# Kernel tuning notes

Hardware: AMD Instinct MI355X
Metric: run time of the kernel (lower is better)

## Reference

```python
import jax, jax.numpy as jnp
import numpy as np

DIM = 384
NUM_HEADS = 12
WS = 8            # window_size
SS = 4            # shift_size
HEAD_DIM = DIM // NUM_HEADS
SCALE = HEAD_DIM ** -0.5
N = WS * WS       # tokens per window
EPS = 1e-5
MLP_HIDDEN = 4 * DIM

# relative position index (static, matches torch buffer construction)
_coords = np.stack(np.meshgrid(np.arange(WS), np.arange(WS), indexing='ij')).reshape(2, -1)
_rel = (_coords[:, :, None] - _coords[:, None, :]).transpose(1, 2, 0)  # [N,N,2]
_rel[..., 0] += WS - 1
_rel[..., 1] += WS - 1
_rel[..., 0] *= 2 * WS - 1
RPI = jnp.asarray(_rel.sum(-1))  # [N,N] int


def layer_norm(x, g, b):
    m = x.mean(-1, keepdims=True)
    v = ((x - m) ** 2).mean(-1, keepdims=True)
    return (x - m) / jnp.sqrt(v + EPS) * g + b


def window_partition(x):
    B, Hh, Ww, C = x.shape
    x = x.reshape(B, Hh // WS, WS, Ww // WS, WS, C).transpose(0, 1, 3, 2, 4, 5)
    return x.reshape(-1, WS, WS, C)


def window_reverse(w, Hh, Ww):
    B = w.shape[0] // ((Hh // WS) * (Ww // WS))
    x = w.reshape(B, Hh // WS, Ww // WS, WS, WS, -1).transpose(0, 1, 3, 2, 4, 5)
    return x.reshape(B, Hh, Ww, -1)


def attention_mask(Hp, Wp):
    # region id along each axis: 0 = [0, Hp-WS), 1 = [Hp-WS, Hp-SS), 2 = [Hp-SS, Hp)
    h_id = np.zeros(Hp, np.int32); h_id[Hp - WS:Hp - SS] = 1; h_id[Hp - SS:] = 2
    w_id = np.zeros(Wp, np.int32); w_id[Wp - WS:Wp - SS] = 1; w_id[Wp - SS:] = 2
    cnt = h_id[:, None] * 3 + w_id[None, :]                      # [Hp, Wp]
    img = jnp.asarray(cnt, jnp.float32).reshape(1, Hp, Wp, 1)
    mw = window_partition(img).reshape(-1, N)                    # [nW, N]
    am = mw[:, None, :] - mw[:, :, None]                         # [nW, N, N]
    return jnp.where(am != 0, jnp.float32(-100.0), jnp.float32(0.0))


def setup_inputs() -> dict:
    key = jax.random.key(0)
    ks = jax.random.split(key, 8)
    B, H, W = 32, 64, 64
    std = 0.02
    return {
        'x': jax.random.normal(ks[0], (B, H * W, DIM), jnp.float32),
        'qkv_w': jax.random.normal(ks[1], (DIM, 3 * DIM), jnp.float32) * std,
        'qkv_b': jnp.zeros((3 * DIM,), jnp.float32),
        'proj_w': jax.random.normal(ks[2], (DIM, DIM), jnp.float32) * std,
        'proj_b': jnp.zeros((DIM,), jnp.float32),
        'rpb_table': jax.random.normal(ks[3], ((2 * WS - 1) * (2 * WS - 1), NUM_HEADS), jnp.float32) * std,
        'n1_g': jnp.ones((DIM,), jnp.float32), 'n1_b': jnp.zeros((DIM,), jnp.float32),
        'n2_g': jnp.ones((DIM,), jnp.float32), 'n2_b': jnp.zeros((DIM,), jnp.float32),
        'fc1_w': jax.random.normal(ks[4], (DIM, MLP_HIDDEN), jnp.float32) * std,
        'fc1_b': jnp.zeros((MLP_HIDDEN,), jnp.float32),
        'fc2_w': jax.random.normal(ks[5], (MLP_HIDDEN, DIM), jnp.float32) * std,
        'fc2_b': jnp.zeros((DIM,), jnp.float32),
        'H': 64, 'W': 64,
    }


def reference(x, qkv_w, qkv_b, proj_w, proj_b, rpb_table, n1_g, n1_b, n2_g, n2_b,
              fc1_w, fc1_b, fc2_w, fc2_b, H, W):
    B, L, C = x.shape
    shortcut = x
    h = layer_norm(x, n1_g, n1_b).reshape(B, H, W, C)
    pad_r = (WS - W % WS) % WS
    pad_b = (WS - H % WS) % WS
    if pad_r or pad_b:
        h = jnp.pad(h, ((0, 0), (0, pad_b), (0, pad_r), (0, 0)))
    Hp, Wp = H + pad_b, W + pad_r
    shifted = jnp.roll(h, shift=(-SS, -SS), axis=(1, 2))
    xw = window_partition(shifted).reshape(-1, N, C)             # [B_, N, C]
    B_ = xw.shape[0]

    qkv = (xw @ qkv_w + qkv_b).reshape(B_, N, 3, NUM_HEADS, HEAD_DIM)
    q = qkv[:, :, 0].transpose(0, 2, 1, 3) * SCALE               # [B_, h, N, d]
    k = qkv[:, :, 1].transpose(0, 2, 1, 3)
    v = qkv[:, :, 2].transpose(0, 2, 1, 3)

    attn = jnp.einsum('bhnd,bhmd->bhnm', q, k)                   # [B_, h, N, N]
    bias = rpb_table[RPI].transpose(2, 0, 1)                     # [h, N, N]
    attn = attn + bias[None]

    mask = attention_mask(Hp, Wp)                                # [nW, N, N]
    nW = mask.shape[0]
    attn = attn.reshape(B_ // nW, nW, NUM_HEADS, N, N) + mask[None, :, None]
    attn = jax.nn.softmax(attn.reshape(B_, NUM_HEADS, N, N), axis=-1)

    out = jnp.einsum('bhnm,bhmd->bhnd', attn, v)
    out = out.transpose(0, 2, 1, 3).reshape(B_, N, C)
    out = out @ proj_w + proj_b

    out = window_reverse(out.reshape(-1, WS, WS, C), Hp, Wp)
    out = jnp.roll(out, shift=(SS, SS), axis=(1, 2))
    out = out[:, :H, :W, :].reshape(B, H * W, C)

    x = shortcut + out
    h2 = layer_norm(x, n2_g, n2_b)
    mlp = jax.nn.gelu(h2 @ fc1_w + fc1_b, approximate=False) @ fc2_w + fc2_b
    return x + mlp
```

## Files before the change

### kernel.cpp

```cpp
#include <hip/hip_runtime.h>
#include <math.h>


#define ROWS_TOTAL 131072
#define NWIN_TOTAL 2048

typedef __attribute__((ext_vector_type(8))) __bf16 bf16x8;
typedef __attribute__((ext_vector_type(4))) float f32x4;
typedef __attribute__((ext_vector_type(8))) unsigned short ushort8;

__device__ __forceinline__ unsigned short f2bf(float f) {
  unsigned u = __builtin_bit_cast(unsigned, f);
  u = (u + 0x7fffu + ((u >> 16) & 1u)) >> 16;
  return (unsigned short)u;
}

__device__ __forceinline__ void gload16(const void* g, void* l) {
  __builtin_amdgcn_global_load_lds(
      (const __attribute__((address_space(1))) unsigned int*)g,
      (__attribute__((address_space(3))) unsigned int*)l, 16, 0, 0);
}

__device__ __forceinline__ int gather_row(int win, int t) {
  int b = win >> 6, wi = (win >> 3) & 7, wj = win & 7;
  int gi = (wi * 8 + (t >> 3) + 4) & 63;
  int gj = (wj * 8 + (t & 7) + 4) & 63;
  return (b << 12) + (gi << 6) + gj;
}

__device__ __forceinline__ void frag_mma(const ushort* As_, const ushort* Bs_,
                                         int wr, int wc, int lane,
                                         f32x4 acc[8][4]) {
  const int go = (((lane >> 4) ^ ((lane >> 1) & 3)) << 3);
  const int lr = lane & 15;
  bf16x8 bfr[4];
#pragma unroll
  for (int nj = 0; nj < 4; ++nj)
    bfr[nj] = *(const bf16x8*)(Bs_ + (wc * 64 + nj * 16 + lr) * 32 + go);
#pragma unroll
  for (int mi = 0; mi < 8; ++mi) {
    bf16x8 af = *(const bf16x8*)(As_ + (wr * 128 + mi * 16 + lr) * 32 + go);
#pragma unroll
    for (int nj = 0; nj < 4; ++nj)
      acc[mi][nj] = __builtin_amdgcn_mfma_f32_16x16x32_bf16(
          af, bfr[nj], acc[mi][nj], 0, 0, 0);
  }
}

#define VM6() asm volatile("s_waitcnt vmcnt(6)" ::: "memory")
#define VM0() asm volatile("s_waitcnt vmcnt(0)" ::: "memory")
#define SCB() __builtin_amdgcn_sched_barrier(0)
#define BARR() __builtin_amdgcn_s_barrier()

#define STG(B_, T_)                                    \
  { size_t ko = (size_t)(T_) * 64;                     \
    gload16(aS0 + ko, &As[B_][aD]);                    \
    gload16(aS1 + ko, &As[B_][aD + 512]);              \
    gload16(aS2 + ko, &As[B_][aD + 1024]);             \
    gload16(aS3 + ko, &As[B_][aD + 1536]);             \
    gload16(bS0 + ko, &Bs[B_][bD]);                    \
    gload16(bS1 + ko, &Bs[B_][bD + 512]); }

#define GEMM_PIPE(NK)                                               \
  {                                                                 \
    STG(0, 0);                                                      \
    STG(1, 1);                                                      \
    VM6(); SCB(); BARR(); SCB();                                    \
    int cur = 0;                                                    \
    for (int t = 0; t < (NK); ++t) {                                \
      if (t + 2 < (NK)) {                                           \
        int nb = cur + 2; if (nb >= 3) nb -= 3;                     \
        STG(nb, t + 2);                                             \
      }                                                             \
      __builtin_amdgcn_s_setprio(1);                                \
      frag_mma(&As[cur][0], &Bs[cur][0], wr, wc, lane, acc);        \
      __builtin_amdgcn_s_setprio(0);                                \
      if (t + 2 < (NK)) { VM6(); } else { VM0(); }                  \
      SCB(); BARR(); SCB();                                         \
      ++cur; if (cur == 3) cur = 0;                                 \
    }                                                               \
  }

__global__ __launch_bounds__(256) void wprep_k(
    const float* __restrict__ qkvw, const float* __restrict__ projw,
    const float* __restrict__ fc1w, const float* __restrict__ fc2w,
    ushort* __restrict__ wq, ushort* __restrict__ wp,
    ushort* __restrict__ w1, ushort* __restrict__ w2) {
  int gid = blockIdx.x * 256 + threadIdx.x;
  const int S1 = 1152 * 384;
  const int S2 = S1 + 384 * 384;
  const int S3 = S2 + 1536 * 384;
  const int S4 = S3 + 384 * 1536;
  if (gid < S1) {
    int n = gid / 384, k = gid - n * 384;
    wq[gid] = f2bf(qkvw[(size_t)k * 1152 + n]);
  } else if (gid < S2) {
    int i = gid - S1, n = i / 384, k = i - n * 384;
    wp[i] = f2bf(projw[(size_t)k * 384 + n]);
  } else if (gid < S3) {
    int i = gid - S2, n = i / 384, k = i - n * 384;
    w1[i] = f2bf(fc1w[(size_t)k * 1536 + n]);
  } else if (gid < S4) {
    int i = gid - S3, n = i / 1536, k = i - n * 1536;
    w2[i] = f2bf(fc2w[(size_t)k * 384 + n]);
  }
}

__global__ __launch_bounds__(256) void ln_fused_k(
    const float* __restrict__ x, const float* __restrict__ g,
    const float* __restrict__ b, ushort* __restrict__ o) {
  int wid = threadIdx.x >> 6, lane = threadIdx.x & 63;
  int row = (blockIdx.x << 2) + wid;
  const float* p = x + (size_t)row * 384;
  float2 v[3];
  float s = 0.f, ss = 0.f;
#pragma unroll
  for (int c = 0; c < 3; ++c) {
    v[c] = *(const float2*)(p + lane * 2 + c * 128);
    s += v[c].x + v[c].y;
    ss += v[c].x * v[c].x + v[c].y * v[c].y;
  }
#pragma unroll
  for (int off = 1; off < 64; off <<= 1) {
    s += __shfl_xor(s, off);
    ss += __shfl_xor(ss, off);
  }
  float m = s * (1.f / 384.f);
  float r = rsqrtf(ss * (1.f / 384.f) - m * m + 1e-5f);
  ushort* op = o + (size_t)row * 384;
#pragma unroll
  for (int c = 0; c < 3; ++c) {
    float2 gg = *(const float2*)(g + lane * 2 + c * 128);
    float2 bb = *(const float2*)(b + lane * 2 + c * 128);
    union { ushort u[2]; unsigned w; } pk;
    pk.u[0] = f2bf((v[c].x - m) * r * gg.x + bb.x);
    pk.u[1] = f2bf((v[c].y - m) * r * gg.y + bb.y);
    *(unsigned*)(op + lane * 2 + c * 128) = pk.w;
  }
}

__global__ __launch_bounds__(256, 2) void qkv_mfma_k(
    const ushort* __restrict__ xln, const ushort* __restrict__ wq,
    const float* __restrict__ qkvb, float* __restrict__ qd,
    float* __restrict__ kd, float* __restrict__ vd, int wc0) {
  __shared__ __align__(16) ushort As[3][8192];
  __shared__ __align__(16) ushort Bs[3][4096];
  __shared__ int rowS[256];
  const int tid = threadIdx.x;
  const int w = tid >> 6, lane = tid & 63;
  const int wr = w >> 1, wc = w & 1;
  const int bm = blockIdx.x, n0 = blockIdx.y * 128;
  {
    int win = wc0 + bm * 4 + (tid >> 6);
    rowS[tid] = gather_row(win, tid & 63);
  }
  __syncthreads();
  const int sle = (((lane & 3) ^ ((lane >> 3) & 3)) << 4);
  const int rb = w * 64 + (lane >> 2);
  const char* aS0 = (const char*)xln + (size_t)rowS[rb] * 768 + sle;
  const char* aS1 = (const char*)xln + (size_t)rowS[rb + 16] * 768 + sle;
  const char* aS2 = (const char*)xln + (size_t)rowS[rb + 32] * 768 + sle;
  const char* aS3 = (const char*)xln + (size_t)rowS[rb + 48] * 768 + sle;
  const int nb = n0 + w * 32 + (lane >> 2);
  const char* bS0 = (const char*)wq + (size_t)nb * 768 + sle;
  const char* bS1 = (const char*)wq + (size_t)(nb + 16) * 768 + sle;
  const int aD = w * 2048 + lane * 8;
  const int bD = w * 1024 + lane * 8;
  f32x4 acc[8][4];
#pragma unroll
  for (int i = 0; i < 8; ++i)
#pragma unroll
    for (int j = 0; j < 4; ++j) acc[i][j] = (f32x4)(0.f);
  GEMM_PIPE(12);
  const float scale = 0.17677669529663687f;
#pragma unroll
  for (int mi = 0; mi < 8; ++mi) {
#pragma unroll
    for (int r = 0; r < 4; ++r) {
      int rr = wr * 128 + mi * 16 + ((lane >> 4) << 2) + r;
      int w_rel = bm * 4 + (rr >> 6), t = rr & 63;
#pragma unroll
      for (int nj = 0; nj < 4; ++nj) {
        int nc = n0 + wc * 64 + nj * 16 + (lane & 15);
        float v = acc[mi][nj][r] + qkvb[nc];
        int qi = nc / 384, rem = nc - qi * 384;
        int hh = rem >> 5, d = rem & 31;
        float* base = (qi == 0) ? qd : (qi == 1 ? kd : vd);
        if (qi == 0) v *= scale;
        base[(((size_t)w_rel * 12 + hh) << 11) + (t << 5) + d] = v;
      }
    }
  }
}

__global__ __launch_bounds__(128) void attn_k(
    const float* __restrict__ q, const float* __restrict__ k,
    const float* __restrict__ v, const float* __restrict__ rpb,
    ushort* __restrict__ ao, int wc0) {
  __shared__ __align__(16) float kbuf[2][64][32];
  __shared__ __align__(16) float vbuf[2][64][32];
  __shared__ float bias[2][232];
  __shared__ int region[64];
  const int tid = threadIdx.x;
  const int wid = tid >> 6, lane = tid & 63;
  const int w = blockIdx.x, win = wc0 + w;
  const int head = blockIdx.y * 2 + wid;
  if (tid < 64) {
    int wi = (win >> 3) & 7, wj = win & 7;
    int pi = wi * 8 + (tid >> 3), pj = wj * 8 + (tid & 7);
    int ri = pi < 56 ? 0 : (pi < 60 ? 1 : 2);
    int rj = pj < 56 ? 0 : (pj < 60 ? 1 : 2);
    region[tid] = ri * 3 + rj;
  }
  const size_t hb = ((size_t)w * 12 + head) * 2048;
  const float* kp = k + hb;
  const float* vp = v + hb;
#pragma unroll
  for (int s = 0; s < 8; ++s) {
    int f = s * 64 + lane;
    int r = f >> 3, c = (f & 7) << 2;
    *(float4*)&kbuf[wid][r][c] = *(const float4*)(kp + r * 32 + c);
    *(float4*)&vbuf[wid][r][c] = *(const float4*)(vp + r * 32 + c);
  }
  for (int s = lane; s < 225; s += 64) bias[wid][s] = rpb[s * 12 + head];
  __syncthreads();
  const int i = lane;
  float qr[32];
  const float* qp = q + hb + (i << 5);
#pragma unroll
  for (int c = 0; c < 32; c += 4) {
    float4 t4 = *(const float4*)(qp + c);
    qr[c] = t4.x; qr[c + 1] = t4.y; qr[c + 2] = t4.z; qr[c + 3] = t4.w;
  }
  const int yi = i >> 3, xi = i & 7, regi = region[i];
  float sc[64];
  float mx = -3.0e38f;
#pragma unroll
  for (int j = 0; j < 64; ++j) {
    float a = 0.f;
#pragma unroll
    for (int c = 0; c < 32; c += 4) {
      float4 kv = *(float4*)&kbuf[wid][j][c];
      a = fmaf(qr[c], kv.x, a);
      a = fmaf(qr[c + 1], kv.y, a);
      a = fmaf(qr[c + 2], kv.z, a);
      a = fmaf(qr[c + 3], kv.w, a);
    }
    int dy = yi - (j >> 3) + 7, dx = xi - (j & 7) + 7;
    a += bias[wid][dy * 15 + dx];
    if (region[j] != regi) a -= 100.f;
    sc[j] = a;
    mx = fmaxf(mx, a);
  }
  float sum = 0.f;
#pragma unroll
  for (int j = 0; j < 64; ++j) {
    float e = __expf(sc[j] - mx);
    sc[j] = e;
    sum += e;
  }
  const float inv = 1.f / sum;
  float o[32];
#pragma unroll
  for (int c = 0; c < 32; ++c) o[c] = 0.f;
#pragma unroll
  for (int j = 0; j < 64; ++j) {
    float p = sc[j];
#pragma unroll
    for (int c = 0; c < 32; c += 4) {
      float4 vv = *(float4*)&vbuf[wid][j][c];
      o[c] = fmaf(p, vv.x, o[c]);
      o[c + 1] = fmaf(p, vv.y, o[c + 1]);
      o[c + 2] = fmaf(p, vv.z, o[c + 2]);
      o[c + 3] = fmaf(p, vv.w, o[c + 3]);
    }
  }
  ushort* op = ao + ((size_t)(w * 64 + i)) * 384 + (head << 5);
#pragma unroll
  for (int c = 0; c < 32; c += 8) {
    ushort8 pk;
#pragma unroll
    for (int j2 = 0; j2 < 8; ++j2) pk[j2] = f2bf(o[c + j2] * inv);
    *(ushort8*)(op + c) = pk;
  }
}

__global__ __launch_bounds__(256, 2) void proj_mfma_k(
    const ushort* __restrict__ ao, const ushort* __restrict__ wp,
    const float* __restrict__ pb, const float* __restrict__ x,
    float* __restrict__ x2, int wc0) {
  __shared__ __align__(16) ushort As[3][8192];
  __shared__ __align__(16) ushort Bs[3][4096];
  const int tid = threadIdx.x;
  const int w = tid >> 6, lane = tid & 63;
  const int wr = w >> 1, wc = w & 1;
  const int bm = blockIdx.x, n0 = blockIdx.y * 128;
  const int sle = (((lane & 3) ^ ((lane >> 3) & 3)) << 4);
  const int rb = bm * 256 + w * 64 + (lane >> 2);
  const char* aS0 = (const char*)ao + (size_t)rb * 768 + sle;
  const char* aS1 = aS0 + (size_t)16 * 768;
  const char* aS2 = aS0 + (size_t)32 * 768;
  const char* aS3 = aS0 + (size_t)48 * 768;
  const int nb = n0 + w * 32 + (lane >> 2);
  const char* bS0 = (const char*)wp + (size_t)nb * 768 + sle;
  const char* bS1 = (const char*)wp + (size_t)(nb + 16) * 768 + sle;
  const int aD = w * 2048 + lane * 8;
  const int bD = w * 1024 + lane * 8;
  f32x4 acc[8][4];
#pragma unroll
  for (int i = 0; i < 8; ++i)
#pragma unroll
    for (int j = 0; j < 4; ++j) acc[i][j] = (f32x4)(0.f);
  GEMM_PIPE(12);
#pragma unroll
  for (int mi = 0; mi < 8; ++mi) {
#pragma unroll
    for (int r = 0; r < 4; ++r) {
      int rr = wr * 128 + mi * 16 + ((lane >> 4) << 2) + r;
      int gl = bm * 256 + rr;
      int gr = gather_row(wc0 + (gl >> 6), gl & 63);
#pragma unroll
      for (int nj = 0; nj < 4; ++nj) {
        int nc = n0 + wc * 64 + nj * 16 + (lane & 15);
        size_t idx = (size_t)gr * 384 + nc;
        x2[idx] = acc[mi][nj][r] + pb[nc] + x[idx];
      }
    }
  }
}

__global__ __launch_bounds__(256, 2) void fc1_mfma_k(
    const ushort* __restrict__ x2ln, const ushort* __restrict__ w1,
    const float* __restrict__ fb, ushort* __restrict__ hm, int row0) {
  __shared__ __align__(16) ushort As[3][8192];
  __shared__ __align__(16) ushort Bs[3][4096];
  const int tid = threadIdx.x;
  const int w = tid >> 6, lane = tid & 63;
  const int wr = w >> 1, wc = w & 1;
  const int bm = blockIdx.x, n0 = blockIdx.y * 128;
  const int sle = (((lane & 3) ^ ((lane >> 3) & 3)) << 4);
  const int rb = row0 + bm * 256 + w * 64 + (lane >> 2);
  const char* aS0 = (const char*)x2ln + (size_t)rb * 768 + sle;
  const char* aS1 = aS0 + (size_t)16 * 768;
  const char* aS2 = aS0 + (size_t)32 * 768;
  const char* aS3 = aS0 + (size_t)48 * 768;
  const int nb = n0 + w * 32 + (lane >> 2);
  const char* bS0 = (const char*)w1 + (size_t)nb * 768 + sle;
  const char* bS1 = (const char*)w1 + (size_t)(nb + 16) * 768 + sle;
  const int aD = w * 2048 + lane * 8;
  const int bD = w * 1024 + lane * 8;
  f32x4 acc[8][4];
#pragma unroll
  for (int i = 0; i < 8; ++i)
#pragma unroll
    for (int j = 0; j < 4; ++j) acc[i][j] = (f32x4)(0.f);
  GEMM_PIPE(12);
#pragma unroll
  for (int mi = 0; mi < 8; ++mi) {
#pragma unroll
    for (int r = 0; r < 4; ++r) {
      int rr = wr * 128 + mi * 16 + ((lane >> 4) << 2) + r;
      size_t lrow = (size_t)(bm * 256 + rr);
#pragma unroll
      for (int nj = 0; nj < 4; ++nj) {
        int nc = n0 + wc * 64 + nj * 16 + (lane & 15);
        float v = acc[mi][nj][r] + fb[nc];
        v = 0.5f * v * (1.f + erff(v * 0.70710678118654752f));
        hm[lrow * 1536 + nc] = f2bf(v);
      }
    }
  }
}

__global__ __launch_bounds__(256, 2) void fc2_mfma_k(
    const ushort* __restrict__ hm, const ushort* __restrict__ w2,
    const float* __restrict__ fb, float* __restrict__ out, int row0) {
  __shared__ __align__(16) ushort As[3][8192];
  __shared__ __align__(16) ushort Bs[3][4096];
  const int tid = threadIdx.x;
  const int w = tid >> 6, lane = tid & 63;
  const int wr = w >> 1, wc = w & 1;
  const int bm = blockIdx.x, n0 = blockIdx.y * 128;
  const int sle = (((lane & 3) ^ ((lane >> 3) & 3)) << 4);
  const int rb = bm * 256 + w * 64 + (lane >> 2);
  const char* aS0 = (const char*)hm + (size_t)rb * 3072 + sle;
  const char* aS1 = aS0 + (size_t)16 * 3072;
  const char* aS2 = aS0 + (size_t)32 * 3072;
  const char* aS3 = aS0 + (size_t)48 * 3072;
  const int nb = n0 + w * 32 + (lane >> 2);
  const char* bS0 = (const char*)w2 + (size_t)nb * 3072 + sle;
  const char* bS1 = (const char*)w2 + (size_t)(nb + 16) * 3072 + sle;
  const int aD = w * 2048 + lane * 8;
  const int bD = w * 1024 + lane * 8;
  f32x4 acc[8][4];
#pragma unroll
  for (int i = 0; i < 8; ++i)
#pragma unroll
    for (int j = 0; j < 4; ++j) acc[i][j] = (f32x4)(0.f);
  GEMM_PIPE(48);
#pragma unroll
  for (int mi = 0; mi < 8; ++mi) {
#pragma unroll
    for (int r = 0; r < 4; ++r) {
      int rr = wr * 128 + mi * 16 + ((lane >> 4) << 2) + r;
      size_t grow = (size_t)(row0 + bm * 256 + rr);
#pragma unroll
      for (int nj = 0; nj < 4; ++nj) {
        int nc = n0 + wc * 64 + nj * 16 + (lane & 15);
        size_t idx = grow * 384 + nc;
        out[idx] = out[idx] + acc[mi][nj][r] + fb[nc];
      }
    }
  }
}

extern "C" void kernel_launch(void* const* d_in, const int* in_sizes, int n_in,
                              void* d_out, int out_size, void* d_ws, size_t ws_size,
                              hipStream_t stream) {
  const float* x = (const float*)d_in[0];
  const float* qkv_w = (const float*)d_in[1];
  const float* qkv_b = (const float*)d_in[2];
  const float* proj_w = (const float*)d_in[3];
  const float* proj_b = (const float*)d_in[4];
  const float* rpb = (const float*)d_in[5];
  const float* n1g = (const float*)d_in[6];
  const float* n1b = (const float*)d_in[7];
  const float* n2g = (const float*)d_in[8];
  const float* n2b = (const float*)d_in[9];
  const float* fc1w = (const float*)d_in[10];
  const float* fc1b = (const float*)d_in[11];
  const float* fc2w = (const float*)d_in[12];
  const float* fc2b = (const float*)d_in[13];
  float* out = (float*)d_out;
  char* ws = (char*)d_ws;

  ushort* wq = (ushort*)ws;
  ushort* wp = wq + 442368;
  ushort* w1 = wp + 147456;
  ushort* w2 = w1 + 589824;
  ushort* xln = (ushort*)(ws + 3538944);
  char* scratch = ws + 3538944 + 100663296;
  size_t base = 3538944 + 100663296;
  size_t ssz = (ws_size > base) ? ws_size - base : 0;

  wprep_k<<<6912, 256, 0, stream>>>(qkv_w, proj_w, fc1w, fc2w, wq, wp, w1, w2);
  ln_fused_k<<<ROWS_TOTAL / 4, 256, 0, stream>>>(x, n1g, n1b, xln);

  const size_t perwin = 344064;
  int nwc = (int)(ssz / perwin);
  if (nwc > NWIN_TOTAL) nwc = NWIN_TOTAL;
  nwc &= ~3;
  if (nwc < 4) nwc = 4;
  float* qd = (float*)scratch;
  float* kd = qd + (size_t)nwc * 24576;
  float* vd = kd + (size_t)nwc * 24576;
  ushort* ao = (ushort*)(vd + (size_t)nwc * 24576);
  for (int wc0 = 0; wc0 < NWIN_TOTAL; wc0 += nwc) {
    int nw = (NWIN_TOTAL - wc0 < nwc) ? (NWIN_TOTAL - wc0) : nwc;
    qkv_mfma_k<<<dim3(nw / 4, 9), 256, 0, stream>>>(xln, wq, qkv_b, qd, kd, vd, wc0);
    attn_k<<<dim3(nw, 6), 128, 0, stream>>>(qd, kd, vd, rpb, ao, wc0);
    proj_mfma_k<<<dim3(nw / 4, 3), 256, 0, stream>>>(ao, wp, proj_b, x, out, wc0);
  }

  ln_fused_k<<<ROWS_TOTAL / 4, 256, 0, stream>>>(out, n2g, n2b, xln);
  const size_t pergrp = 786432;
  int ngc = (int)(ssz / pergrp);
  if (ngc > 512) ngc = 512;
  if (ngc < 1) ngc = 1;
  ushort* hm = (ushort*)scratch;
  for (int g0 = 0; g0 < 512; g0 += ngc) {
    int ng = (512 - g0 < ngc) ? (512 - g0) : ngc;
    fc1_mfma_k<<<dim3(ng, 12), 256, 0, stream>>>(xln, w1, fc1b, hm, g0 * 256);
    fc2_mfma_k<<<dim3(ng, 3), 256, 0, stream>>>(hm, w2, fc2b, out, g0 * 256);
  }
}
```

Measured before the change: 1.600 ms.

## Load GEMM fragments directly from global into registers; store QKV as bf16

Replaces the LDS triple-buffered global_load_lds pipeline in all four GEMMs with direct per-lane global loads of MFMA fragments into registers, double-buffered over K steps. Stores Q/K/V intermediates as bf16 instead of fp32, halving scratch traffic and letting more windows fit per chunk. Swaps the grid dimensions so N-tiles vary fastest, which should improve reuse of the A operand in L2. The risks are that dropping LDS sharing means each wave fetches its own operands from global/L2 with less coalescing, that register pressure rises, and that bf16 Q/K/V slightly reduces precision.

```diff
diff --git a/kernel.cpp b/kernel.cpp
--- a/kernel.cpp
+++ b/kernel.cpp
@@ -14,11 +14,8 @@
   u = (u + 0x7fffu + ((u >> 16) & 1u)) >> 16;
   return (unsigned short)u;
 }
-
-__device__ __forceinline__ void gload16(const void* g, void* l) {
-  __builtin_amdgcn_global_load_lds(
-      (const __attribute__((address_space(1))) unsigned int*)g,
-      (__attribute__((address_space(3))) unsigned int*)l, 16, 0, 0);
+__device__ __forceinline__ float bf2f(unsigned short u) {
+  return __builtin_bit_cast(float, (unsigned)u << 16);
 }
 
 __device__ __forceinline__ int gather_row(int win, int t) {
@@ -28,57 +25,45 @@
   return (b << 12) + (gi << 6) + gj;
 }
 
-__device__ __forceinline__ void frag_mma(const ushort* As_, const ushort* Bs_,
-                                         int wr, int wc, int lane,
-                                         f32x4 acc[8][4]) {
-  const int go = (((lane >> 4) ^ ((lane >> 1) & 3)) << 3);
-  const int lr = lane & 15;
-  bf16x8 bfr[4];
-#pragma unroll
-  for (int nj = 0; nj < 4; ++nj)
-    bfr[nj] = *(const bf16x8*)(Bs_ + (wc * 64 + nj * 16 + lr) * 32 + go);
-#pragma unroll
-  for (int mi = 0; mi < 8; ++mi) {
-    bf16x8 af = *(const bf16x8*)(As_ + (wr * 128 + mi * 16 + lr) * 32 + go);
-#pragma unroll
-    for (int nj = 0; nj < 4; ++nj)
-      acc[mi][nj] = __builtin_amdgcn_mfma_f32_16x16x32_bf16(
-          af, bfr[nj], acc[mi][nj], 0, 0, 0);
-  }
-}
-
-#define VM6() asm volatile("s_waitcnt vmcnt(6)" ::: "memory")
-#define VM0() asm volatile("s_waitcnt vmcnt(0)" ::: "memory")
-#define SCB() __builtin_amdgcn_sched_barrier(0)
-#define BARR() __builtin_amdgcn_s_barrier()
-
-#define STG(B_, T_)                                    \
-  { size_t ko = (size_t)(T_) * 64;                     \
-    gload16(aS0 + ko, &As[B_][aD]);                    \
-    gload16(aS1 + ko, &As[B_][aD + 512]);              \
-    gload16(aS2 + ko, &As[B_][aD + 1024]);             \
-    gload16(aS3 + ko, &As[B_][aD + 1536]);             \
-    gload16(bS0 + ko, &Bs[B_][bD]);                    \
-    gload16(bS1 + ko, &Bs[B_][bD + 512]); }
-
-#define GEMM_PIPE(NK)                                               \
-  {                                                                 \
-    STG(0, 0);                                                      \
-    STG(1, 1);                                                      \
-    VM6(); SCB(); BARR(); SCB();                                    \
-    int cur = 0;                                                    \
-    for (int t = 0; t < (NK); ++t) {                                \
-      if (t + 2 < (NK)) {                                           \
-        int nb = cur + 2; if (nb >= 3) nb -= 3;                     \
-        STG(nb, t + 2);                                             \
-      }                                                             \
-      __builtin_amdgcn_s_setprio(1);                                \
-      frag_mma(&As[cur][0], &Bs[cur][0], wr, wc, lane, acc);        \
-      __builtin_amdgcn_s_setprio(0);                                \
-      if (t + 2 < (NK)) { VM6(); } else { VM0(); }                  \
-      SCB(); BARR(); SCB();                                         \
-      ++cur; if (cur == 3) cur = 0;                                 \
-    }                                                               \
+#define MFMA_SET(AF, BF)                                                   \
+  _Pragma("unroll") for (int mi = 0; mi < 8; ++mi)                         \
+  _Pragma("unroll") for (int nj = 0; nj < 4; ++nj)                         \
+      acc[mi][nj] = __builtin_amdgcn_mfma_f32_16x16x32_bf16(               \
+          AF[mi], BF[nj], acc[mi][nj], 0, 0, 0);
+
+#define REG_PIPE(NK)                                                       \
+  {                                                                        \
+    bf16x8 a0[8], b0[4], a1[8], b1[4];                                     \
+    _Pragma("unroll") for (int i = 0; i < 8; ++i)                          \
+        a0[i] = *(const bf16x8*)aP[i];                                     \
+    _Pragma("unroll") for (int j = 0; j < 4; ++j)                          \
+        b0[j] = *(const bf16x8*)bP[j];                                     \
+    _Pragma("unroll") for (int i = 0; i < 8; ++i)                          \
+        a1[i] = *(const bf16x8*)(aP[i] + 32);                              \
+    _Pragma("unroll") for (int j = 0; j < 4; ++j)                          \
+        b1[j] = *(const bf16x8*)(bP[j] + 32);                              \
+    for (int t = 0; t < (NK) - 2; t += 2) {                                \
+      _Pragma("unroll") for (int i = 0; i < 8; ++i) aP[i] += 64;           \
+      _Pragma("unroll") for (int j = 0; j < 4; ++j) bP[j] += 64;           \
+      __builtin_amdgcn_s_setprio(1);                                       \
+      MFMA_SET(a0, b0);                                                    \
+      __builtin_amdgcn_s_setprio(0);                                       \
+      _Pragma("unroll") for (int i = 0; i < 8; ++i)                        \
+          a0[i] = *(const bf16x8*)aP[i];                                   \
+      _Pragma("unroll") for (int j = 0; j < 4; ++j)                        \
+          b0[j] = *(const bf16x8*)bP[j];                                   \
+      __builtin_amdgcn_s_setprio(1);                                       \
+      MFMA_SET(a1, b1);                                                    \
+      __builtin_amdgcn_s_setprio(0);                                       \
+      _Pragma("unroll") for (int i = 0; i < 8; ++i)                        \
+          a1[i] = *(const bf16x8*)(aP[i] + 32);                            \
+      _Pragma("unroll") for (int j = 0; j < 4; ++j)                        \
+          b1[j] = *(const bf16x8*)(bP[j] + 32);                            \
+    }                                                                      \
+    __builtin_amdgcn_s_setprio(1);                                         \
+    MFMA_SET(a0, b0);                                                      \
+    MFMA_SET(a1, b1);                                                      \
+    __builtin_amdgcn_s_setprio(0);                                         \
   }
 
 __global__ __launch_bounds__(256) void wprep_k(
@@ -141,37 +126,30 @@
 
 __global__ __launch_bounds__(256, 2) void qkv_mfma_k(
     const ushort* __restrict__ xln, const ushort* __restrict__ wq,
-    const float* __restrict__ qkvb, float* __restrict__ qd,
-    float* __restrict__ kd, float* __restrict__ vd, int wc0) {
-  __shared__ __align__(16) ushort As[3][8192];
-  __shared__ __align__(16) ushort Bs[3][4096];
-  __shared__ int rowS[256];
+    const float* __restrict__ qkvb, ushort* __restrict__ qd,
+    ushort* __restrict__ kd, ushort* __restrict__ vd, int wc0) {
   const int tid = threadIdx.x;
   const int w = tid >> 6, lane = tid & 63;
   const int wr = w >> 1, wc = w & 1;
-  const int bm = blockIdx.x, n0 = blockIdx.y * 128;
-  {
-    int win = wc0 + bm * 4 + (tid >> 6);
-    rowS[tid] = gather_row(win, tid & 63);
-  }
-  __syncthreads();
-  const int sle = (((lane & 3) ^ ((lane >> 3) & 3)) << 4);
-  const int rb = w * 64 + (lane >> 2);
-  const char* aS0 = (const char*)xln + (size_t)rowS[rb] * 768 + sle;
-  const char* aS1 = (const char*)xln + (size_t)rowS[rb + 16] * 768 + sle;
-  const char* aS2 = (const char*)xln + (size_t)rowS[rb + 32] * 768 + sle;
-  const char* aS3 = (const char*)xln + (size_t)rowS[rb + 48] * 768 + sle;
-  const int nb = n0 + w * 32 + (lane >> 2);
-  const char* bS0 = (const char*)wq + (size_t)nb * 768 + sle;
-  const char* bS1 = (const char*)wq + (size_t)(nb + 16) * 768 + sle;
-  const int aD = w * 2048 + lane * 8;
-  const int bD = w * 1024 + lane * 8;
+  const int n0 = blockIdx.x * 128, bm = blockIdx.y;
+  const int lr = lane & 15, kch = (lane >> 4) * 8;
+  const ushort* aP[8];
+#pragma unroll
+  for (int i = 0; i < 8; ++i) {
+    int rr = wr * 128 + i * 16 + lr;
+    int gr = gather_row(wc0 + bm * 4 + (rr >> 6), rr & 63);
+    aP[i] = xln + (size_t)gr * 384 + kch;
+  }
+  const ushort* bP[4];
+#pragma unroll
+  for (int j = 0; j < 4; ++j)
+    bP[j] = wq + (size_t)(n0 + wc * 64 + j * 16 + lr) * 384 + kch;
   f32x4 acc[8][4];
 #pragma unroll
   for (int i = 0; i < 8; ++i)
 #pragma unroll
     for (int j = 0; j < 4; ++j) acc[i][j] = (f32x4)(0.f);
-  GEMM_PIPE(12);
+  REG_PIPE(12);
   const float scale = 0.17677669529663687f;
 #pragma unroll
   for (int mi = 0; mi < 8; ++mi) {
@@ -185,17 +163,17 @@
         float v = acc[mi][nj][r] + qkvb[nc];
         int qi = nc / 384, rem = nc - qi * 384;
         int hh = rem >> 5, d = rem & 31;
-        float* base = (qi == 0) ? qd : (qi == 1 ? kd : vd);
+        ushort* base = (qi == 0) ? qd : (qi == 1 ? kd : vd);
         if (qi == 0) v *= scale;
-        base[(((size_t)w_rel * 12 + hh) << 11) + (t << 5) + d] = v;
+        base[(((size_t)w_rel * 12 + hh) << 11) + (t << 5) + d] = f2bf(v);
       }
     }
   }
 }
 
 __global__ __launch_bounds__(128) void attn_k(
-    const float* __restrict__ q, const float* __restrict__ k,
-    const float* __restrict__ v, const float* __restrict__ rpb,
+    const ushort* __restrict__ q, const ushort* __restrict__ k,
+    const ushort* __restrict__ v, const float* __restrict__ rpb,
     ushort* __restrict__ ao, int wc0) {
   __shared__ __align__(16) float kbuf[2][64][32];
   __shared__ __align__(16) float vbuf[2][64][32];
@@ -213,24 +191,30 @@
     region[tid] = ri * 3 + rj;
   }
   const size_t hb = ((size_t)w * 12 + head) * 2048;
-  const float* kp = k + hb;
-  const float* vp = v + hb;
-#pragma unroll
-  for (int s = 0; s < 8; ++s) {
+  const ushort* kp = k + hb;
+  const ushort* vp = v + hb;
+#pragma unroll
+  for (int s = 0; s < 4; ++s) {
     int f = s * 64 + lane;
-    int r = f >> 3, c = (f & 7) << 2;
-    *(float4*)&kbuf[wid][r][c] = *(const float4*)(kp + r * 32 + c);
-    *(float4*)&vbuf[wid][r][c] = *(const float4*)(vp + r * 32 + c);
+    int r = f >> 2, c = (f & 3) * 8;
+    ushort8 ku = *(const ushort8*)(kp + r * 32 + c);
+    ushort8 vu = *(const ushort8*)(vp + r * 32 + c);
+#pragma unroll
+    for (int j = 0; j < 8; ++j) {
+      kbuf[wid][r][c + j] = bf2f(ku[j]);
+      vbuf[wid][r][c + j] = bf2f(vu[j]);
+    }
   }
   for (int s = lane; s < 225; s += 64) bias[wid][s] = rpb[s * 12 + head];
   __syncthreads();
   const int i = lane;
   float qr[32];
-  const float* qp = q + hb + (i << 5);
-#pragma unroll
-  for (int c = 0; c < 32; c += 4) {
-    float4 t4 = *(const float4*)(qp + c);
-    qr[c] = t4.x; qr[c + 1] = t4.y; qr[c + 2] = t4.z; qr[c + 3] = t4.w;
+  const ushort* qp = q + hb + (i << 5);
+#pragma unroll
+  for (int c = 0; c < 4; ++c) {
+    ushort8 qu = *(const ushort8*)(qp + c * 8);
+#pragma unroll
+    for (int j = 0; j < 8; ++j) qr[c * 8 + j] = bf2f(qu[j]);
   }
   const int yi = i >> 3, xi = i & 7, regi = region[i];
   float sc[64];
@@ -289,29 +273,25 @@
     const ushort* __restrict__ ao, const ushort* __restrict__ wp,
     const float* __restrict__ pb, const float* __restrict__ x,
     float* __restrict__ x2, int wc0) {
-  __shared__ __align__(16) ushort As[3][8192];
-  __shared__ __align__(16) ushort Bs[3][4096];
   const int tid = threadIdx.x;
   const int w = tid >> 6, lane = tid & 63;
   const int wr = w >> 1, wc = w & 1;
-  const int bm = blockIdx.x, n0 = blockIdx.y * 128;
-  const int sle = (((lane & 3) ^ ((lane >> 3) & 3)) << 4);
-  const int rb = bm * 256 + w * 64 + (lane >> 2);
-  const char* aS0 = (const char*)ao + (size_t)rb * 768 + sle;
-  const char* aS1 = aS0 + (size_t)16 * 768;
-  const char* aS2 = aS0 + (size_t)32 * 768;
-  const char* aS3 = aS0 + (size_t)48 * 768;
-  const int nb = n0 + w * 32 + (lane >> 2);
-  const char* bS0 = (const char*)wp + (size_t)nb * 768 + sle;
-  const char* bS1 = (const char*)wp + (size_t)(nb + 16) * 768 + sle;
-  const int aD = w * 2048 + lane * 8;
-  const int bD = w * 1024 + lane * 8;
+  const int n0 = blockIdx.x * 128, bm = blockIdx.y;
+  const int lr = lane & 15, kch = (lane >> 4) * 8;
+  const ushort* aP[8];
+#pragma unroll
+  for (int i = 0; i < 8; ++i)
+    aP[i] = ao + (size_t)(bm * 256 + wr * 128 + i * 16 + lr) * 384 + kch;
+  const ushort* bP[4];
+#pragma unroll
+  for (int j = 0; j < 4; ++j)
+    bP[j] = wp + (size_t)(n0 + wc * 64 + j * 16 + lr) * 384 + kch;
   f32x4 acc[8][4];
 #pragma unroll
   for (int i = 0; i < 8; ++i)
 #pragma unroll
     for (int j = 0; j < 4; ++j) acc[i][j] = (f32x4)(0.f);
-  GEMM_PIPE(12);
+  REG_PIPE(12);
 #pragma unroll
   for (int mi = 0; mi < 8; ++mi) {
 #pragma unroll
@@ -332,29 +312,25 @@
 __global__ __launch_bounds__(256, 2) void fc1_mfma_k(
     const ushort* __restrict__ x2ln, const ushort* __restrict__ w1,
     const float* __restrict__ fb, ushort* __restrict__ hm, int row0) {
-  __shared__ __align__(16) ushort As[3][8192];
-  __shared__ __align__(16) ushort Bs[3][4096];
   const int tid = threadIdx.x;
   const int w = tid >> 6, lane = tid & 63;
   const int wr = w >> 1, wc = w & 1;
-  const int bm = blockIdx.x, n0 = blockIdx.y * 128;
-  const int sle = (((lane & 3) ^ ((lane >> 3) & 3)) << 4);
-  const int rb = row0 + bm * 256 + w * 64 + (lane >> 2);
-  const char* aS0 = (const char*)x2ln + (size_t)rb * 768 + sle;
-  const char* aS1 = aS0 + (size_t)16 * 768;
-  const char* aS2 = aS0 + (size_t)32 * 768;
-  const char* aS3 = aS0 + (size_t)48 * 768;
-  const int nb = n0 + w * 32 + (lane >> 2);
-  const char* bS0 = (const char*)w1 + (size_t)nb * 768 + sle;
-  const char* bS1 = (const char*)w1 + (size_t)(nb + 16) * 768 + sle;
-  const int aD = w * 2048 + lane * 8;
-  const int bD = w * 1024 + lane * 8;
+  const int n0 = blockIdx.x * 128, bm = blockIdx.y;
+  const int lr = lane & 15, kch = (lane >> 4) * 8;
+  const ushort* aP[8];
+#pragma unroll
+  for (int i = 0; i < 8; ++i)
+    aP[i] = x2ln + (size_t)(row0 + bm * 256 + wr * 128 + i * 16 + lr) * 384 + kch;
+  const ushort* bP[4];
+#pragma unroll
+  for (int j = 0; j < 4; ++j)
+    bP[j] = w1 + (size_t)(n0 + wc * 64 + j * 16 + lr) * 384 + kch;
   f32x4 acc[8][4];
 #pragma unroll
   for (int i = 0; i < 8; ++i)
 #pragma unroll
     for (int j = 0; j < 4; ++j) acc[i][j] = (f32x4)(0.f);
-  GEMM_PIPE(12);
+  REG_PIPE(12);
 #pragma unroll
   for (int mi = 0; mi < 8; ++mi) {
 #pragma unroll
@@ -364,9 +340,9 @@
 #pragma unroll
       for (int nj = 0; nj < 4; ++nj) {
         int nc = n0 + wc * 64 + nj * 16 + (lane & 15);
-        float v = acc[mi][nj][r] + fb[nc];
-        v = 0.5f * v * (1.f + erff(v * 0.70710678118654752f));
-        hm[lrow * 1536 + nc] = f2bf(v);
+        float vv = acc[mi][nj][r] + fb[nc];
+        vv = 0.5f * vv * (1.f + erff(vv * 0.70710678118654752f));
+        hm[lrow * 1536 + nc] = f2bf(vv);
       }
     }
   }
@@ -375,29 +351,25 @@
 __global__ __launch_bounds__(256, 2) void fc2_mfma_k(
     const ushort* __restrict__ hm, const ushort* __restrict__ w2,
     const float* __restrict__ fb, float* __restrict__ out, int row0) {
-  __shared__ __align__(16) ushort As[3][8192];
-  __shared__ __align__(16) ushort Bs[3][4096];
   const int tid = threadIdx.x;
   const int w = tid >> 6, lane = tid & 63;
   const int wr = w >> 1, wc = w & 1;
-  const int bm = blockIdx.x, n0 = blockIdx.y * 128;
-  const int sle = (((lane & 3) ^ ((lane >> 3) & 3)) << 4);
-  const int rb = bm * 256 + w * 64 + (lane >> 2);
-  const char* aS0 = (const char*)hm + (size_t)rb * 3072 + sle;
-  const char* aS1 = aS0 + (size_t)16 * 3072;
-  const char* aS2 = aS0 + (size_t)32 * 3072;
-  const char* aS3 = aS0 + (size_t)48 * 3072;
-  const int nb = n0 + w * 32 + (lane >> 2);
-  const char* bS0 = (const char*)w2 + (size_t)nb * 3072 + sle;
-  const char* bS1 = (const char*)w2 + (size_t)(nb + 16) * 3072 + sle;
-  const int aD = w * 2048 + lane * 8;
-  const int bD = w * 1024 + lane * 8;
+  const int n0 = blockIdx.x * 128, bm = blockIdx.y;
+  const int lr = lane & 15, kch = (lane >> 4) * 8;
+  const ushort* aP[8];
+#pragma unroll
+  for (int i = 0; i < 8; ++i)
+    aP[i] = hm + (size_t)(bm * 256 + wr * 128 + i * 16 + lr) * 1536 + kch;
+  const ushort* bP[4];
+#pragma unroll
+  for (int j = 0; j < 4; ++j)
+    bP[j] = w2 + (size_t)(n0 + wc * 64 + j * 16 + lr) * 1536 + kch;
   f32x4 acc[8][4];
 #pragma unroll
   for (int i = 0; i < 8; ++i)
 #pragma unroll
     for (int j = 0; j < 4; ++j) acc[i][j] = (f32x4)(0.f);
-  GEMM_PIPE(48);
+  REG_PIPE(48);
 #pragma unroll
   for (int mi = 0; mi < 8; ++mi) {
 #pragma unroll
@@ -446,20 +418,20 @@
   wprep_k<<<6912, 256, 0, stream>>>(qkv_w, proj_w, fc1w, fc2w, wq, wp, w1, w2);
   ln_fused_k<<<ROWS_TOTAL / 4, 256, 0, stream>>>(x, n1g, n1b, xln);
 
-  const size_t perwin = 344064;
+  const size_t perwin = 196608;
   int nwc = (int)(ssz / perwin);
   if (nwc > NWIN_TOTAL) nwc = NWIN_TOTAL;
   nwc &= ~3;
   if (nwc < 4) nwc = 4;
-  float* qd = (float*)scratch;
-  float* kd = qd + (size_t)nwc * 24576;
-  float* vd = kd + (size_t)nwc * 24576;
-  ushort* ao = (ushort*)(vd + (size_t)nwc * 24576);
+  ushort* qd = (ushort*)scratch;
+  ushort* kd = qd + (size_t)nwc * 24576;
+  ushort* vd = kd + (size_t)nwc * 24576;
+  ushort* ao = vd + (size_t)nwc * 24576;
   for (int wc0 = 0; wc0 < NWIN_TOTAL; wc0 += nwc) {
     int nw = (NWIN_TOTAL - wc0 < nwc) ? (NWIN_TOTAL - wc0) : nwc;
-    qkv_mfma_k<<<dim3(nw / 4, 9), 256, 0, stream>>>(xln, wq, qkv_b, qd, kd, vd, wc0);
+    qkv_mfma_k<<<dim3(9, nw / 4), 256, 0, stream>>>(xln, wq, qkv_b, qd, kd, vd, wc0);
     attn_k<<<dim3(nw, 6), 128, 0, stream>>>(qd, kd, vd, rpb, ao, wc0);
-    proj_mfma_k<<<dim3(nw / 4, 3), 256, 0, stream>>>(ao, wp, proj_b, x, out, wc0);
+    proj_mfma_k<<<dim3(3, nw / 4), 256, 0, stream>>>(ao, wp, proj_b, x, out, wc0);
   }
 
   ln_fused_k<<<ROWS_TOTAL / 4, 256, 0, stream>>>(out, n2g, n2b, xln);
@@ -470,7 +442,7 @@
   ushort* hm = (ushort*)scratch;
   for (int g0 = 0; g0 < 512; g0 += ngc) {
     int ng = (512 - g0 < ngc) ? (512 - g0) : ngc;
-    fc1_mfma_k<<<dim3(ng, 12), 256, 0, stream>>>(xln, w1, fc1b, hm, g0 * 256);
-    fc2_mfma_k<<<dim3(ng, 3), 256, 0, stream>>>(hm, w2, fc2b, out, g0 * 256);
-  }
-}
+    fc1_mfma_k<<<dim3(12, ng), 256, 0, stream>>>(xln, w1, fc1b, hm, g0 * 256);
+    fc2_mfma_k<<<dim3(3, ng), 256, 0, stream>>>(hm, w2, fc2b, out, g0 * 256);
+  }
+}
```

New measurement: 2.079 ms. +29.9%, slower.
